# Performance work log

Measured on AMD Instinct MI355X. Metric: run time of the kernel, lower is better.

The kernel has to match this reference:

```python
import jax, jax.numpy as jnp
import numpy as np

B, CN, DEG, IN_F, OUT_F, K = 32, 1024, 2, 128, 128, 10
NODES = [1, 16, 128, 1024]


def setup_inputs() -> dict:
    key = jax.random.key(0)
    ks = jax.random.split(key, 16)
    d = {}
    for i, n in enumerate(NODES):
        d[f"tree{i}"] = jax.random.normal(ks[i], (B, n, IN_F), dtype=jnp.float32)
    for i in range(4):
        d[f"Uw{i}"] = jax.random.normal(ks[4 + i], (IN_F, OUT_F), dtype=jnp.float32) * 0.05
        d[f"Ub{i}"] = jnp.zeros((OUT_F,), dtype=jnp.float32)
    d["W_up"] = jax.random.normal(ks[8], (CN, IN_F, DEG * IN_F), dtype=jnp.float32) * 0.05
    d["Fw0"] = jax.random.normal(ks[9], (IN_F, K * IN_F), dtype=jnp.float32) * 0.05
    d["Fb0"] = jnp.zeros((K * IN_F,), dtype=jnp.float32)
    d["Fw1"] = jax.random.normal(ks[10], (K * IN_F, OUT_F), dtype=jnp.float32) * 0.05
    d["Fb1"] = jnp.zeros((OUT_F,), dtype=jnp.float32)
    d["b_bias"] = jax.random.normal(ks[11], (1, DEG * CN, OUT_F), dtype=jnp.float32) * 0.05
    return d


def reference(tree0, tree1, tree2, tree3,
              Uw0, Ub0, Uw1, Ub1, Uw2, Ub2, Uw3, Ub3,
              W_up, Fw0, Fb0, Fw1, Fb1, b_bias):
    tree = [tree0, tree1, tree2, tree3]
    Uw = [Uw0, Uw1, Uw2, Uw3]
    Ub = [Ub0, Ub1, Ub2, Ub3]
    curr_node = W_up.shape[0]
    in_feat = W_up.shape[1]
    degree = W_up.shape[2] // in_feat

    # Ancestor info: project each depth, then tile each ancestor node's
    # projected vector to cover its descendants at the current level.
    anc = jnp.zeros((tree[0].shape[0], curr_node, Uw0.shape[1]), dtype=tree0.dtype)
    for t, w, b in zip(tree, Uw, Ub):
        Q = t @ w + b                       # [B, anc_node, out_feat]
        rep = curr_node // t.shape[1]
        anc = anc + jnp.repeat(Q, rep, axis=1)  # == tf.tile([1,1,rep]) + reshape

    # Per-node unique-weight upsample: [B,n,1,in] @ [n,in,deg*in]
    nl = jnp.einsum('bni,nio->bno', tree[-1], W_up)            # [B, CN, deg*in]
    nl = nl.reshape(nl.shape[0], curr_node * degree, in_feat)   # [B, CN*deg, in]
    nl = (nl @ Fw0 + Fb0) @ Fw1 + Fb1                           # Dense chain
    nl = nl + jnp.repeat(anc, degree, axis=1)                   # broadcast ancestors
    nl = nl + b_bias
    return jnp.where(nl >= 0, nl, 0.2 * nl)                     # LeakyReLU(0.2)
```

## Files before the change

kernel.cpp:

```cpp
#include <hip/hip_runtime.h>
#include <stdint.h>


using short8   = __attribute__((ext_vector_type(8))) short;
using floatx16 = __attribute__((ext_vector_type(16))) float;

__device__ __forceinline__ unsigned short f2bf(float f) {
    unsigned int u = __builtin_bit_cast(unsigned int, f);
    return (unsigned short)((u + 0x8000u) >> 16);
}

#define QS_OFF  0
#define FB_OFF  524288
#define FF_OFF  524416
#define UW_OFF  532608

__global__ __launch_bounds__(256) void ffused_p1(
    const float* __restrict__ Fw0, const float* __restrict__ Fb0,
    const float* __restrict__ Fw1, float* __restrict__ P)
{
    const int kc = blockIdx.x;
    const int i  = blockIdx.y;
    const int j  = threadIdx.x & 127;
    const int il = threadIdx.x >> 7;
    const int k0 = kc * 160 + il * 80;
    const float* __restrict__ src = (i < 128) ? (Fw0 + (size_t)i * 1280) : Fb0;
    float acc = 0.f;
    #pragma unroll 8
    for (int kk = 0; kk < 80; ++kk)
        acc += src[k0 + kk] * Fw1[(size_t)(k0 + kk) * 128 + j];
    P[(size_t)(kc * 2 + il) * 16512 + i * 128 + j] = acc;
}

__global__ __launch_bounds__(256) void ffused_p2(
    const float* __restrict__ P, const float* __restrict__ Fb1,
    unsigned short* __restrict__ FfusedBF, float* __restrict__ Fbias)
{
    const int idx = blockIdx.x * 256 + threadIdx.x;
    if (idx >= 16512) return;
    const int i = idx >> 7, j = idx & 127;
    float s = 0.f;
    #pragma unroll
    for (int p = 0; p < 16; ++p) s += P[(size_t)p * 16512 + idx];
    if (i < 128) FfusedBF[(((i >> 3) * 128) + j) * 8 + (i & 7)] = f2bf(s);
    else         Fbias[j] = s + Fb1[j];
}

__global__ __launch_bounds__(256) void uwbf_kernel(
    const float* __restrict__ Uw0, const float* __restrict__ Uw1,
    const float* __restrict__ Uw2, const float* __restrict__ Uw3,
    unsigned short* __restrict__ UwBF)
{
    const int mat = blockIdx.x >> 4;
    const int kg  = blockIdx.x & 15;
    const float* __restrict__ Uw = (mat == 0) ? Uw0 : (mat == 1) ? Uw1
                                 : (mat == 2) ? Uw2 : Uw3;
    const int col = threadIdx.x & 127;
    const int kh  = threadIdx.x >> 7;
    #pragma unroll
    for (int q = 0; q < 4; ++q) {
        const int kk = kh * 4 + q;
        const float v = Uw[(size_t)(kg * 8 + kk) * 128 + col];
        UwBF[(((size_t)(mat * 16 + kg) * 128) + col) * 8 + kk] = f2bf(v);
    }
}

__global__ __launch_bounds__(256) void qsum_kernel(
    const float* __restrict__ t0, const float* __restrict__ t1,
    const float* __restrict__ t2, const unsigned short* __restrict__ UwBF,
    float* __restrict__ Qsum)
{
    const int i2   = blockIdx.x;
    const int tid  = threadIdx.x;
    const int w    = tid >> 6;
    const int lane = tid & 63;
    const int l31  = lane & 31;
    const int half = lane >> 5;
    const int colq = w * 32 + l31;

    __shared__ __align__(16) unsigned short Alds[48 * 33 * 8];

    #pragma unroll
    for (int mi = 0; mi < 3; ++mi) {
        const float* __restrict__ base = (mi == 0) ? t0 : (mi == 1) ? t1 : t2;
        #pragma unroll
        for (int i = 0; i < 4; ++i) {
            const int idx = i * 256 + tid;
            const int b   = idx >> 5;
            const int q   = idx & 31;
            int row;
            if      (mi == 0) row = b;
            else if (mi == 1) row = b * 16 + (i2 >> 3);
            else              row = b * 128 + i2;
            const float4 v = *reinterpret_cast<const float4*>(
                base + (size_t)row * 128 + q * 4);
            ushort4 u;
            u.x = f2bf(v.x); u.y = f2bf(v.y); u.z = f2bf(v.z); u.w = f2bf(v.w);
            const int kg = mi * 16 + (q >> 1);
            *reinterpret_cast<ushort4*>(&Alds[(kg * 33 + b) * 8 + (q & 1) * 4]) = u;
        }
    }
    __syncthreads();

    floatx16 acc;
    #pragma unroll
    for (int r = 0; r < 16; ++r) acc[r] = 0.f;
    #pragma unroll
    for (int ks = 0; ks < 24; ++ks) {
        const int kg = 2 * ks + half;
        const short8 a = *reinterpret_cast<const short8*>(&Alds[(kg * 33 + l31) * 8]);
        const short8 bf = *reinterpret_cast<const short8*>(
            &UwBF[(((size_t)kg * 128) + colq) * 8]);
        acc = __builtin_amdgcn_mfma_f32_32x32x16_bf16(a, bf, acc, 0, 0, 0);
    }
    #pragma unroll
    for (int r = 0; r < 16; ++r) {
        const int brow = (r & 3) + 8 * (r >> 2) + 4 * half;
        Qsum[((size_t)i2 * 32 + brow) * 128 + colq] = acc[r];
    }
}

__global__ __launch_bounds__(256, 2) void tree_main(
    const float* __restrict__ t3,
    const float* __restrict__ Ub0, const float* __restrict__ Ub1,
    const float* __restrict__ Ub2, const float* __restrict__ Ub3,
    const float* __restrict__ Wup, const float* __restrict__ bbias,
    const unsigned short* __restrict__ FfusedBF,
    const unsigned short* __restrict__ UwBF,
    const float* __restrict__ Fbias, const float* __restrict__ Qsum,
    float* __restrict__ out)
{
    const int n    = blockIdx.x;
    const int tid  = threadIdx.x;
    const int w    = tid >> 6;
    const int lane = tid & 63;
    const int l31  = lane & 31;
    const int half = lane >> 5;
    const int colq = w * 32 + l31;

    __shared__ __align__(16) unsigned char smem_raw[16640];
    unsigned short* T3lds = (unsigned short*)smem_raw;
    unsigned short* Ulds  = (unsigned short*)smem_raw;

    #pragma unroll
    for (int i = 0; i < 4; ++i) {
        const int idx = i * 256 + tid;
        const int b   = idx >> 5;
        const int q   = idx & 31;
        const float4 v = *reinterpret_cast<const float4*>(
            t3 + ((size_t)b * 1024 + n) * 128 + q * 4);
        ushort4 u;
        u.x = f2bf(v.x); u.y = f2bf(v.y); u.z = f2bf(v.z); u.w = f2bf(v.w);
        *reinterpret_cast<ushort4*>(&T3lds[((q >> 1) * 33 + b) * 8 + (q & 1) * 4]) = u;
    }
    __syncthreads();

    floatx16 qacc, accT0, accT1;
    #pragma unroll
    for (int r = 0; r < 16; ++r) { qacc[r] = 0.f; accT0[r] = 0.f; accT1[r] = 0.f; }

    const float* __restrict__ Wp0 = Wup + (size_t)n * 32768 + (half * 8) * 256 + w * 64 + l31;
    const float* __restrict__ Wp1 = Wp0 + 32;

    float p0[8], p1[8];
    #pragma unroll
    for (int jj = 0; jj < 8; ++jj) { p0[jj] = Wp0[jj * 256]; p1[jj] = Wp1[jj * 256]; }

    #pragma unroll
    for (int ks = 0; ks < 8; ++ks) {
        float n0[8], n1[8];
        if (ks < 7) {
            const int koff = (ks + 1) * 16 * 256;
            #pragma unroll
            for (int jj = 0; jj < 8; ++jj) {
                n0[jj] = Wp0[koff + jj * 256];
                n1[jj] = Wp1[koff + jj * 256];
            }
        }
        const short8 afk = *reinterpret_cast<const short8*>(
            &T3lds[((2 * ks + half) * 33 + l31) * 8]);
        const short8 bfu = *reinterpret_cast<const short8*>(
            &UwBF[(((size_t)(48 + 2 * ks + half) * 128) + colq) * 8]);
        short8 a0, a1;
        #pragma unroll
        for (int jj = 0; jj < 8; ++jj) {
            a0[jj] = (short)f2bf(p0[jj]);
            a1[jj] = (short)f2bf(p1[jj]);
        }
        qacc  = __builtin_amdgcn_mfma_f32_32x32x16_bf16(afk, bfu, qacc, 0, 0, 0);
        accT0 = __builtin_amdgcn_mfma_f32_32x32x16_bf16(a0, afk, accT0, 0, 0, 0);
        accT1 = __builtin_amdgcn_mfma_f32_32x32x16_bf16(a1, afk, accT1, 0, 0, 0);
        #pragma unroll
        for (int jj = 0; jj < 8; ++jj) { p0[jj] = n0[jj]; p1[jj] = n1[jj]; }
    }
    __syncthreads();

    #pragma unroll
    for (int tt = 0; tt < 2; ++tt) {
        const floatx16 Av = tt ? accT1 : accT0;
        #pragma unroll
        for (int r = 0; r < 16; ++r) {
            const int cm = w * 64 + tt * 32 + ((r & 3) + 8 * (r >> 2) + 4 * half);
            const int d  = cm >> 7;
            const int cp = cm & 127;
            Ulds[(((cp >> 3) * 65) + d * 32 + l31) * 8 + (cp & 7)] = f2bf(Av[r]);
        }
    }
    __syncthreads();

    const int i2 = n >> 3;
    float qs[16];
    #pragma unroll
    for (int r = 0; r < 16; ++r) {
        const int brow = (r & 3) + 8 * (r >> 2) + 4 * half;
        qs[r] = Qsum[((size_t)i2 * 32 + brow) * 128 + colq];
    }
    const float ubsum = Ub0[colq] + Ub1[colq] + Ub2[colq] + Ub3[colq] + Fbias[colq];
    const float bb0 = bbias[(size_t)(2 * n + 0) * 128 + colq];
    const float bb1 = bbias[(size_t)(2 * n + 1) * 128 + colq];

    floatx16 o0, o1;
    #pragma unroll
    for (int r = 0; r < 16; ++r) { o0[r] = 0.f; o1[r] = 0.f; }
    #pragma unroll
    for (int ks = 0; ks < 8; ++ks) {
        const int kg2 = 2 * ks + half;
        const short8 a0 = *reinterpret_cast<const short8*>(&Ulds[(kg2 * 65 + l31) * 8]);
        const short8 a1 = *reinterpret_cast<const short8*>(&Ulds[(kg2 * 65 + 32 + l31) * 8]);
        const short8 bf = *reinterpret_cast<const short8*>(
            &FfusedBF[(((size_t)kg2 * 128) + colq) * 8]);
        o0 = __builtin_amdgcn_mfma_f32_32x32x16_bf16(a0, bf, o0, 0, 0, 0);
        o1 = __builtin_amdgcn_mfma_f32_32x32x16_bf16(a1, bf, o1, 0, 0, 0);
    }

    #pragma unroll
    for (int r = 0; r < 16; ++r) {
        const int brow = (r & 3) + 8 * (r >> 2) + 4 * half;
        const float addc = qacc[r] + ubsum + qs[r];
        float v0 = o0[r] + addc + bb0;
        float v1 = o1[r] + addc + bb1;
        v0 = (v0 >= 0.f) ? v0 : 0.2f * v0;
        v1 = (v1 >= 0.f) ? v1 : 0.2f * v1;
        const size_t idx0 = ((size_t)brow * 2048 + 2 * n) * 128 + colq;
        out[idx0]       = v0;
        out[idx0 + 128] = v1;
    }
}

extern "C" void kernel_launch(void* const* d_in, const int* in_sizes, int n_in,
                              void* d_out, int out_size, void* d_ws, size_t ws_size,
                              hipStream_t stream) {
    const float* t0  = (const float*)d_in[0];
    const float* t1  = (const float*)d_in[1];
    const float* t2  = (const float*)d_in[2];
    const float* t3  = (const float*)d_in[3];
    const float* Uw0 = (const float*)d_in[4];
    const float* Ub0 = (const float*)d_in[5];
    const float* Uw1 = (const float*)d_in[6];
    const float* Ub1 = (const float*)d_in[7];
    const float* Uw2 = (const float*)d_in[8];
    const float* Ub2 = (const float*)d_in[9];
    const float* Uw3 = (const float*)d_in[10];
    const float* Ub3 = (const float*)d_in[11];
    const float* Wup = (const float*)d_in[12];
    const float* Fw0 = (const float*)d_in[13];
    const float* Fb0 = (const float*)d_in[14];
    const float* Fw1 = (const float*)d_in[15];
    const float* Fb1 = (const float*)d_in[16];
    const float* bb  = (const float*)d_in[17];

    float* ws = (float*)d_ws;
    float* Qsum           = ws + QS_OFF;
    float* Fbias          = ws + FB_OFF;
    unsigned short* FfBF  = (unsigned short*)(ws + FF_OFF);
    unsigned short* UwBF  = (unsigned short*)(ws + UW_OFF);

    ffused_p1<<<dim3(8, 129), 256, 0, stream>>>(Fw0, Fb0, Fw1, Qsum);
    ffused_p2<<<65, 256, 0, stream>>>(Qsum, Fb1, FfBF, Fbias);
    uwbf_kernel<<<64, 256, 0, stream>>>(Uw0, Uw1, Uw2, Uw3, UwBF);
    qsum_kernel<<<128, 256, 0, stream>>>(t0, t1, t2, UwBF, Qsum);
    tree_main<<<1024, 256, 0, stream>>>(t3,
                                        Ub0, Ub1, Ub2, Ub3,
                                        Wup, bb, FfBF, UwBF, Fbias, Qsum,
                                        (float*)d_out);
}
```

Baseline: 268.1 us.

## Fold ancestor projection into main kernel and merge prep kernels

Removes the separate qsum kernel by having each tree_main block load t0..t2 rows and compute the full ancestor projection itself. The two small prep kernels are merged into one launch, cutting the total from five launches to three. All W_up weight loads are now issued up front in four register sets instead of being software-pipelined one step ahead. In exchange each of the 1024 blocks repeats ancestor MFMA work that 128 blocks did before, uses more LDS and registers, and the deeper prefetch risks register pressure under the two-blocks-per-CU launch bound.

```diff
diff --git a/kernel.cpp b/kernel.cpp
--- a/kernel.cpp
+++ b/kernel.cpp
@@ -10,7 +10,6 @@
     return (unsigned short)((u + 0x8000u) >> 16);
 }
 
-#define QS_OFF  0
 #define FB_OFF  524288
 #define FF_OFF  524416
 #define UW_OFF  532608
@@ -32,102 +31,48 @@
     P[(size_t)(kc * 2 + il) * 16512 + i * 128 + j] = acc;
 }
 
-__global__ __launch_bounds__(256) void ffused_p2(
+__global__ __launch_bounds__(256) void prep2(
     const float* __restrict__ P, const float* __restrict__ Fb1,
-    unsigned short* __restrict__ FfusedBF, float* __restrict__ Fbias)
-{
-    const int idx = blockIdx.x * 256 + threadIdx.x;
-    if (idx >= 16512) return;
-    const int i = idx >> 7, j = idx & 127;
-    float s = 0.f;
-    #pragma unroll
-    for (int p = 0; p < 16; ++p) s += P[(size_t)p * 16512 + idx];
-    if (i < 128) FfusedBF[(((i >> 3) * 128) + j) * 8 + (i & 7)] = f2bf(s);
-    else         Fbias[j] = s + Fb1[j];
-}
-
-__global__ __launch_bounds__(256) void uwbf_kernel(
     const float* __restrict__ Uw0, const float* __restrict__ Uw1,
     const float* __restrict__ Uw2, const float* __restrict__ Uw3,
+    unsigned short* __restrict__ FfusedBF, float* __restrict__ Fbias,
     unsigned short* __restrict__ UwBF)
 {
-    const int mat = blockIdx.x >> 4;
-    const int kg  = blockIdx.x & 15;
-    const float* __restrict__ Uw = (mat == 0) ? Uw0 : (mat == 1) ? Uw1
-                                 : (mat == 2) ? Uw2 : Uw3;
-    const int col = threadIdx.x & 127;
-    const int kh  = threadIdx.x >> 7;
-    #pragma unroll
-    for (int q = 0; q < 4; ++q) {
-        const int kk = kh * 4 + q;
-        const float v = Uw[(size_t)(kg * 8 + kk) * 128 + col];
-        UwBF[(((size_t)(mat * 16 + kg) * 128) + col) * 8 + kk] = f2bf(v);
-    }
-}
-
-__global__ __launch_bounds__(256) void qsum_kernel(
+    if (blockIdx.x < 65) {
+        const int idx = blockIdx.x * 256 + threadIdx.x;
+        if (idx >= 16512) return;
+        const int i = idx >> 7, j = idx & 127;
+        float s = 0.f;
+        #pragma unroll
+        for (int p = 0; p < 16; ++p) s += P[(size_t)p * 16512 + idx];
+        if (i < 128) FfusedBF[(((i >> 3) * 128) + j) * 8 + (i & 7)] = f2bf(s);
+        else         Fbias[j] = s + Fb1[j];
+    } else {
+        const int bx  = blockIdx.x - 65;
+        const int mat = bx >> 4;
+        const int kg  = bx & 15;
+        const float* __restrict__ Uw = (mat == 0) ? Uw0 : (mat == 1) ? Uw1
+                                     : (mat == 2) ? Uw2 : Uw3;
+        const int col = threadIdx.x & 127;
+        const int kh  = threadIdx.x >> 7;
+        #pragma unroll
+        for (int q = 0; q < 4; ++q) {
+            const int kk = kh * 4 + q;
+            const float v = Uw[(size_t)(kg * 8 + kk) * 128 + col];
+            UwBF[(((size_t)(mat * 16 + kg) * 128) + col) * 8 + kk] = f2bf(v);
+        }
+    }
+}
+
+__global__ __launch_bounds__(256, 2) void tree_main(
     const float* __restrict__ t0, const float* __restrict__ t1,
-    const float* __restrict__ t2, const unsigned short* __restrict__ UwBF,
-    float* __restrict__ Qsum)
-{
-    const int i2   = blockIdx.x;
-    const int tid  = threadIdx.x;
-    const int w    = tid >> 6;
-    const int lane = tid & 63;
-    const int l31  = lane & 31;
-    const int half = lane >> 5;
-    const int colq = w * 32 + l31;
-
-    __shared__ __align__(16) unsigned short Alds[48 * 33 * 8];
-
-    #pragma unroll
-    for (int mi = 0; mi < 3; ++mi) {
-        const float* __restrict__ base = (mi == 0) ? t0 : (mi == 1) ? t1 : t2;
-        #pragma unroll
-        for (int i = 0; i < 4; ++i) {
-            const int idx = i * 256 + tid;
-            const int b   = idx >> 5;
-            const int q   = idx & 31;
-            int row;
-            if      (mi == 0) row = b;
-            else if (mi == 1) row = b * 16 + (i2 >> 3);
-            else              row = b * 128 + i2;
-            const float4 v = *reinterpret_cast<const float4*>(
-                base + (size_t)row * 128 + q * 4);
-            ushort4 u;
-            u.x = f2bf(v.x); u.y = f2bf(v.y); u.z = f2bf(v.z); u.w = f2bf(v.w);
-            const int kg = mi * 16 + (q >> 1);
-            *reinterpret_cast<ushort4*>(&Alds[(kg * 33 + b) * 8 + (q & 1) * 4]) = u;
-        }
-    }
-    __syncthreads();
-
-    floatx16 acc;
-    #pragma unroll
-    for (int r = 0; r < 16; ++r) acc[r] = 0.f;
-    #pragma unroll
-    for (int ks = 0; ks < 24; ++ks) {
-        const int kg = 2 * ks + half;
-        const short8 a = *reinterpret_cast<const short8*>(&Alds[(kg * 33 + l31) * 8]);
-        const short8 bf = *reinterpret_cast<const short8*>(
-            &UwBF[(((size_t)kg * 128) + colq) * 8]);
-        acc = __builtin_amdgcn_mfma_f32_32x32x16_bf16(a, bf, acc, 0, 0, 0);
-    }
-    #pragma unroll
-    for (int r = 0; r < 16; ++r) {
-        const int brow = (r & 3) + 8 * (r >> 2) + 4 * half;
-        Qsum[((size_t)i2 * 32 + brow) * 128 + colq] = acc[r];
-    }
-}
-
-__global__ __launch_bounds__(256, 2) void tree_main(
-    const float* __restrict__ t3,
+    const float* __restrict__ t2, const float* __restrict__ t3,
     const float* __restrict__ Ub0, const float* __restrict__ Ub1,
     const float* __restrict__ Ub2, const float* __restrict__ Ub3,
     const float* __restrict__ Wup, const float* __restrict__ bbias,
     const unsigned short* __restrict__ FfusedBF,
     const unsigned short* __restrict__ UwBF,
-    const float* __restrict__ Fbias, const float* __restrict__ Qsum,
+    const float* __restrict__ Fbias,
     float* __restrict__ out)
 {
     const int n    = blockIdx.x;
@@ -137,21 +82,42 @@
     const int l31  = lane & 31;
     const int half = lane >> 5;
     const int colq = w * 32 + l31;
-
-    __shared__ __align__(16) unsigned char smem_raw[16640];
-    unsigned short* T3lds = (unsigned short*)smem_raw;
-    unsigned short* Ulds  = (unsigned short*)smem_raw;
-
-    #pragma unroll
-    for (int i = 0; i < 4; ++i) {
-        const int idx = i * 256 + tid;
-        const int b   = idx >> 5;
-        const int q   = idx & 31;
-        const float4 v = *reinterpret_cast<const float4*>(
-            t3 + ((size_t)b * 1024 + n) * 128 + q * 4);
-        ushort4 u;
-        u.x = f2bf(v.x); u.y = f2bf(v.y); u.z = f2bf(v.z); u.w = f2bf(v.w);
-        *reinterpret_cast<ushort4*>(&T3lds[((q >> 1) * 33 + b) * 8 + (q & 1) * 4]) = u;
+    const int i2   = n >> 3;
+
+    __shared__ __align__(16) unsigned char smem_raw[64 * 33 * 8 * 2];
+    unsigned short* Alds = (unsigned short*)smem_raw;
+    unsigned short* Ulds = (unsigned short*)smem_raw;
+
+    const float* __restrict__ Wbase =
+        Wup + (size_t)n * 32768 + (half * 8) * 256 + w * 64 + l31;
+    float Wa0[8], Wa1[8], Wb0[8], Wb1[8], Wc0[8], Wc1[8], Wd0[8], Wd1[8];
+#define LOADW(P0, P1, WT) \
+    { const float* __restrict__ wp = Wbase + (WT) * 16 * 256; \
+      _Pragma("unroll") \
+      for (int jj = 0; jj < 8; ++jj) { P0[jj] = wp[jj * 256]; P1[jj] = wp[32 + jj * 256]; } }
+    LOADW(Wa0, Wa1, 0) LOADW(Wb0, Wb1, 1) LOADW(Wc0, Wc1, 2) LOADW(Wd0, Wd1, 3)
+
+    #pragma unroll
+    for (int mi = 0; mi < 4; ++mi) {
+        const float* __restrict__ base = (mi == 0) ? t0 : (mi == 1) ? t1
+                                       : (mi == 2) ? t2 : t3;
+        #pragma unroll
+        for (int i = 0; i < 4; ++i) {
+            const int idx = i * 256 + tid;
+            const int b   = idx >> 5;
+            const int q   = idx & 31;
+            int row;
+            if      (mi == 0) row = b;
+            else if (mi == 1) row = b * 16 + (i2 >> 3);
+            else if (mi == 2) row = b * 128 + i2;
+            else              row = b * 1024 + n;
+            const float4 v = *reinterpret_cast<const float4*>(
+                base + (size_t)row * 128 + q * 4);
+            ushort4 u;
+            u.x = f2bf(v.x); u.y = f2bf(v.y); u.z = f2bf(v.z); u.w = f2bf(v.w);
+            *reinterpret_cast<ushort4*>(
+                &Alds[((mi * 16 + (q >> 1)) * 33 + b) * 8 + (q & 1) * 4]) = u;
+        }
     }
     __syncthreads();
 
@@ -159,40 +125,37 @@
     #pragma unroll
     for (int r = 0; r < 16; ++r) { qacc[r] = 0.f; accT0[r] = 0.f; accT1[r] = 0.f; }
 
-    const float* __restrict__ Wp0 = Wup + (size_t)n * 32768 + (half * 8) * 256 + w * 64 + l31;
-    const float* __restrict__ Wp1 = Wp0 + 32;
-
-    float p0[8], p1[8];
-    #pragma unroll
-    for (int jj = 0; jj < 8; ++jj) { p0[jj] = Wp0[jj * 256]; p1[jj] = Wp1[jj * 256]; }
-
-    #pragma unroll
-    for (int ks = 0; ks < 8; ++ks) {
-        float n0[8], n1[8];
-        if (ks < 7) {
-            const int koff = (ks + 1) * 16 * 256;
-            #pragma unroll
-            for (int jj = 0; jj < 8; ++jj) {
-                n0[jj] = Wp0[koff + jj * 256];
-                n1[jj] = Wp1[koff + jj * 256];
-            }
-        }
-        const short8 afk = *reinterpret_cast<const short8*>(
-            &T3lds[((2 * ks + half) * 33 + l31) * 8]);
-        const short8 bfu = *reinterpret_cast<const short8*>(
-            &UwBF[(((size_t)(48 + 2 * ks + half) * 128) + colq) * 8]);
-        short8 a0, a1;
-        #pragma unroll
-        for (int jj = 0; jj < 8; ++jj) {
-            a0[jj] = (short)f2bf(p0[jj]);
-            a1[jj] = (short)f2bf(p1[jj]);
-        }
-        qacc  = __builtin_amdgcn_mfma_f32_32x32x16_bf16(afk, bfu, qacc, 0, 0, 0);
-        accT0 = __builtin_amdgcn_mfma_f32_32x32x16_bf16(a0, afk, accT0, 0, 0, 0);
-        accT1 = __builtin_amdgcn_mfma_f32_32x32x16_bf16(a1, afk, accT1, 0, 0, 0);
-        #pragma unroll
-        for (int jj = 0; jj < 8; ++jj) { p0[jj] = n0[jj]; p1[jj] = n1[jj]; }
-    }
+    #pragma unroll
+    for (int ks = 0; ks < 24; ++ks) {
+        const int kg = 2 * ks + half;
+        const short8 a  = *reinterpret_cast<const short8*>(&Alds[(kg * 33 + l31) * 8]);
+        const short8 bf = *reinterpret_cast<const short8*>(
+            &UwBF[((size_t)kg * 128 + colq) * 8]);
+        qacc = __builtin_amdgcn_mfma_f32_32x32x16_bf16(a, bf, qacc, 0, 0, 0);
+    }
+
+#define WBODY(P0, P1, WT) \
+    { const int kg = 48 + 2 * (WT) + half; \
+      const short8 a  = *reinterpret_cast<const short8*>(&Alds[(kg * 33 + l31) * 8]); \
+      const short8 bf = *reinterpret_cast<const short8*>( \
+          &UwBF[((size_t)kg * 128 + colq) * 8]); \
+      qacc = __builtin_amdgcn_mfma_f32_32x32x16_bf16(a, bf, qacc, 0, 0, 0); \
+      short8 a0, a1; \
+      _Pragma("unroll") \
+      for (int jj = 0; jj < 8; ++jj) { \
+          a0[jj] = (short)f2bf(P0[jj]); a1[jj] = (short)f2bf(P1[jj]); } \
+      accT0 = __builtin_amdgcn_mfma_f32_32x32x16_bf16(a0, a, accT0, 0, 0, 0); \
+      accT1 = __builtin_amdgcn_mfma_f32_32x32x16_bf16(a1, a, accT1, 0, 0, 0); }
+
+    WBODY(Wa0, Wa1, 0) LOADW(Wa0, Wa1, 4)
+    WBODY(Wb0, Wb1, 1) LOADW(Wb0, Wb1, 5)
+    WBODY(Wc0, Wc1, 2) LOADW(Wc0, Wc1, 6)
+    WBODY(Wd0, Wd1, 3) LOADW(Wd0, Wd1, 7)
+    WBODY(Wa0, Wa1, 4)
+    WBODY(Wb0, Wb1, 5)
+    WBODY(Wc0, Wc1, 6)
+    WBODY(Wd0, Wd1, 7)
+
     __syncthreads();
 
     #pragma unroll
@@ -208,13 +171,6 @@
     }
     __syncthreads();
 
-    const int i2 = n >> 3;
-    float qs[16];
-    #pragma unroll
-    for (int r = 0; r < 16; ++r) {
-        const int brow = (r & 3) + 8 * (r >> 2) + 4 * half;
-        qs[r] = Qsum[((size_t)i2 * 32 + brow) * 128 + colq];
-    }
     const float ubsum = Ub0[colq] + Ub1[colq] + Ub2[colq] + Ub3[colq] + Fbias[colq];
     const float bb0 = bbias[(size_t)(2 * n + 0) * 128 + colq];
     const float bb1 = bbias[(size_t)(2 * n + 1) * 128 + colq];
@@ -236,7 +192,7 @@
     #pragma unroll
     for (int r = 0; r < 16; ++r) {
         const int brow = (r & 3) + 8 * (r >> 2) + 4 * half;
-        const float addc = qacc[r] + ubsum + qs[r];
+        const float addc = qacc[r] + ubsum;
         float v0 = o0[r] + addc + bb0;
         float v1 = o1[r] + addc + bb1;
         v0 = (v0 >= 0.f) ? v0 : 0.2f * v0;
@@ -270,17 +226,15 @@
     const float* bb  = (const float*)d_in[17];
 
     float* ws = (float*)d_ws;
-    float* Qsum           = ws + QS_OFF;
+    float* P              = ws;
     float* Fbias          = ws + FB_OFF;
     unsigned short* FfBF  = (unsigned short*)(ws + FF_OFF);
     unsigned short* UwBF  = (unsigned short*)(ws + UW_OFF);
 
-    ffused_p1<<<dim3(8, 129), 256, 0, stream>>>(Fw0, Fb0, Fw1, Qsum);
-    ffused_p2<<<65, 256, 0, stream>>>(Qsum, Fb1, FfBF, Fbias);
-    uwbf_kernel<<<64, 256, 0, stream>>>(Uw0, Uw1, Uw2, Uw3, UwBF);
-    qsum_kernel<<<128, 256, 0, stream>>>(t0, t1, t2, UwBF, Qsum);
-    tree_main<<<1024, 256, 0, stream>>>(t3,
+    ffused_p1<<<dim3(8, 129), 256, 0, stream>>>(Fw0, Fb0, Fw1, P);
+    prep2<<<129, 256, 0, stream>>>(P, Fb1, Uw0, Uw1, Uw2, Uw3, FfBF, Fbias, UwBF);
+    tree_main<<<1024, 256, 0, stream>>>(t0, t1, t2, t3,
                                         Ub0, Ub1, Ub2, Ub3,
-                                        Wup, bb, FfBF, UwBF, Fbias, Qsum,
-                                        (float*)d_out);
-}
+                                        Wup, bb, FfBF, UwBF,
+                                        Fbias, (float*)d_out);
+}
```

Result: no change. 264.7 us, median of 2 (-1.3%).
